# Kernel tuning notes

Measured on AMD Instinct MI355X. Metric: run time of the kernel, lower is better.

Reference implementation:

```python
import jax, jax.numpy as jnp
import numpy as np

N, E, IN_DIM, HIDDEN, OUT_DIM, HOPS, NUM_GRAPHS = 50000, 800000, 128, 128, 10, 4, 128


def setup_inputs() -> dict:
    key = jax.random.key(0)
    ks = jax.random.split(key, 10)
    x = jax.random.normal(ks[0], (N, IN_DIM), dtype=jnp.float32)
    edge_index = jax.random.randint(ks[1], (2, E), 0, N, dtype=jnp.int64)
    batch = jnp.sort(jax.random.randint(ks[2], (N,), 0, NUM_GRAPHS, dtype=jnp.int64))
    s = 0.05
    W_in = jax.random.normal(ks[3], (IN_DIM, HIDDEN), dtype=jnp.float32) * s
    b_in = jnp.zeros((HIDDEN,), dtype=jnp.float32)
    W_hops = jax.random.normal(ks[4], (HOPS, HIDDEN, HIDDEN), dtype=jnp.float32) * s
    b_hops = jnp.zeros((HOPS, HIDDEN), dtype=jnp.float32)
    W_cls = jax.random.normal(ks[5], (HIDDEN, OUT_DIM), dtype=jnp.float32) * s
    b_cls = jnp.zeros((OUT_DIM,), dtype=jnp.float32)
    return {"x": x, "edge_index": edge_index, "batch": batch,
            "W_in": W_in, "b_in": b_in, "W_hops": W_hops, "b_hops": b_hops,
            "W_cls": W_cls, "b_cls": b_cls}


def reference(x, edge_index, batch, W_in, b_in, W_hops, b_hops, W_cls, b_cls):
    src, dst = edge_index[0], edge_index[1]
    # LinearEncoder
    h = x @ W_in + b_in
    # GCN symmetric normalization with self-loops (edge weight 1):
    # deg[i] = 1 + in-degree(i)
    deg = 1.0 + jax.ops.segment_sum(jnp.ones((E,), h.dtype), dst, num_segments=N)
    dinv = deg ** -0.5                      # [N]
    edge_norm = (dinv[src] * dinv[dst])[:, None]   # [E,1]
    self_norm = (dinv * dinv)[:, None]             # [N,1]

    def gcn_conv(h, W, b):
        xw = h @ W                                           # [N,H]
        msg = xw[src] * edge_norm                            # gather + scale
        agg = jax.ops.segment_sum(msg, dst, num_segments=N)  # scatter-add
        return agg + xw * self_norm + b

    for i in range(HOPS):
        h = gcn_conv(h, W_hops[i], b_hops[i])
        if i != HOPS - 1:
            h = jax.nn.relu(h)  # dropout is identity in eval mode

    y = h @ W_cls + b_cls                                    # [N,OUT]
    # global mean pool over graphs
    sums = jax.ops.segment_sum(y, batch, num_segments=NUM_GRAPHS)
    cnts = jax.ops.segment_sum(jnp.ones((N,), y.dtype), batch, num_segments=NUM_GRAPHS)
    return sums / jnp.maximum(cnts, 1.0)[:, None]
```

## Files before the change

### kernel.cpp

```cpp
#include <hip/hip_runtime.h>
#include <hip/hip_fp16.h>

#define N_NODES 50000
#define N_EDGES 800000
#define HID 128
#define OUTD 10
#define NGRAPH 128
#define CAP 64
#define OVF_MAX 4096
#define GBM 64
#define EPT 2

typedef __attribute__((ext_vector_type(8))) short short8;
typedef __attribute__((ext_vector_type(4))) float f32x4;

__device__ __forceinline__ int ld_idx(const int* p, int i, int is64) {
  return is64 ? p[2 * i] : p[i];
}

__device__ __forceinline__ void split1(float v, unsigned& hb, unsigned& lb) {
  unsigned u = __float_as_uint(v);
  hb = (u + 0x7FFFu + ((u >> 16) & 1u)) >> 16;
  float r = v - __uint_as_float(hb << 16);
  unsigned ur = __float_as_uint(r);
  lb = (ur + 0x7FFFu + ((ur >> 16) & 1u)) >> 16;
}

__device__ __forceinline__ float4 h4_to_f4(uint2 u) {
  __half2 a = *(__half2*)&u.x;
  __half2 b = *(__half2*)&u.y;
  float2 fa = __half22float2(a);
  float2 fb = __half22float2(b);
  return make_float4(fa.x, fa.y, fb.x, fb.y);
}

__global__ __launch_bounds__(256) void setup_kernel(const int* __restrict__ ei,
                                                    const float* __restrict__ W_in,
                                                    const float* __restrict__ W_hops,
                                                    const float* __restrict__ Wc,
                                                    const float* __restrict__ b4,
                                                    const float* __restrict__ bc,
                                                    int* __restrict__ flag,
                                                    unsigned short* __restrict__ WhiT,
                                                    unsigned short* __restrict__ WloT,
                                                    float* __restrict__ Wf,
                                                    float* __restrict__ bf) {
  int b = blockIdx.x;
  int tid = threadIdx.x;
  if (b == 0) {
    if (tid == 0) {
      int all0 = 1;
      for (int i = 0; i < 64; ++i) {
        if (ei[2 * i + 1] != 0) { all0 = 0; break; }
      }
      flag[0] = all0;
    }
  } else if (b <= 4) {
    int m = b - 1;
    const float* W = (m == 0) ? W_in : (W_hops + (size_t)(m - 1) * HID * HID);
    unsigned short* oh = WhiT + (size_t)m * HID * HID;
    unsigned short* ol = WloT + (size_t)m * HID * HID;
    for (int it = 0; it < 64; ++it) {
      int idx = it * 256 + tid;
      int k = idx >> 7, n = idx & 127;
      unsigned hb, lb;
      split1(W[k * HID + n], hb, lb);
      oh[n * HID + k] = (unsigned short)hb;
      ol[n * HID + k] = (unsigned short)lb;
    }
  } else {
    const float* W4 = W_hops + 3 * (size_t)HID * HID;
    for (int idx = tid; idx < HID * OUTD; idx += 256) {
      int k = idx / OUTD, o = idx % OUTD;
      float s = 0.f;
      for (int j = 0; j < HID; ++j) s += W4[k * HID + j] * Wc[j * OUTD + o];
      Wf[idx] = s;
    }
    if (tid < OUTD) {
      float s = bc[tid];
      for (int j = 0; j < HID; ++j) s += b4[j] * Wc[j * OUTD + tid];
      bf[tid] = s;
    }
  }
}

__global__ __launch_bounds__(256) void ew_kernel(const int* __restrict__ fillcnt,
                                                 const int* __restrict__ col_fixed,
                                                 float* __restrict__ ew) {
  int wave = threadIdx.x >> 6;
  int lane = threadIdx.x & 63;
  int node = blockIdx.x * 4 + wave;
  if (node >= N_NODES) return;
  int deg = fillcnt[node];
  float dd = 1.0f / sqrtf(1.0f + (float)deg);
  int m = min(deg, CAP);
  if (lane < m) {
    int src = col_fixed[node * CAP + lane];
    float ds = 1.0f / sqrtf(1.0f + (float)fillcnt[src]);
    ew[node * CAP + lane] = dd * ds;
  }
}

__device__ __forceinline__ void gemm_mfma_body(const float* __restrict__ A,
                                               const unsigned short* __restrict__ WhT,
                                               const unsigned short* __restrict__ WlT,
                                               const float* __restrict__ bias,
                                               float* __restrict__ C32,
                                               __half* __restrict__ C16,
                                               int M, int row0) {
  __shared__ unsigned short sBall[2 * 64 * HID];
  unsigned short* sBhi = sBall;
  unsigned short* sBlo = sBall + 64 * HID;
  int tid = threadIdx.x;
  int w = tid >> 6, lane = tid & 63;
  int m = lane & 15, kq = lane >> 4;
  int arow = min(row0 + w * 16 + m, M - 1);
  const float* Ap = A + (size_t)arow * HID + kq * 8;

  short8 AH[4], AL[4];
#pragma unroll
  for (int kc4 = 0; kc4 < 4; ++kc4) {
    float4 a0 = *(const float4*)(Ap + kc4 * 32);
    float4 a1 = *(const float4*)(Ap + kc4 * 32 + 4);
    float av[8] = {a0.x, a0.y, a0.z, a0.w, a1.x, a1.y, a1.z, a1.w};
#pragma unroll
    for (int i = 0; i < 8; ++i) {
      unsigned hb, lb;
      split1(av[i], hb, lb);
      AH[kc4][i] = (short)hb;
      AL[kc4][i] = (short)lb;
    }
  }

  f32x4 acc[8];
#pragma unroll
  for (int j = 0; j < 8; ++j) acc[j] = (f32x4){0.f, 0.f, 0.f, 0.f};

#pragma unroll
  for (int half = 0; half < 2; ++half) {
    if (half) __syncthreads();
#pragma unroll
    for (int it = 0; it < 8; ++it) {
      int f = it * 256 + tid;
      int mat = f >> 10;
      int ln = (f >> 4) & 63;
      int c = f & 15;
      int cs = c ^ (ln & 15);
      const unsigned short* src = (mat ? WlT : WhT) + (size_t)(half * 64 + ln) * HID + c * 8;
      unsigned short* dst = (mat ? sBlo : sBhi) + ln * HID + cs * 8;
      *(uint4*)dst = *(const uint4*)src;
    }
    __syncthreads();

#pragma unroll
    for (int kc4 = 0; kc4 < 4; ++kc4) {
      int kc = kc4 * 4 + kq;
      int cs = kc ^ m;
#pragma unroll
      for (int jl = 0; jl < 4; ++jl) {
        int ln = jl * 16 + m;
        short8 bhi = *(const short8*)&sBhi[ln * HID + cs * 8];
        short8 blo = *(const short8*)&sBlo[ln * HID + cs * 8];
        int j = half * 4 + jl;
        acc[j] = __builtin_amdgcn_mfma_f32_16x16x32_bf16(AH[kc4], bhi, acc[j], 0, 0, 0);
        acc[j] = __builtin_amdgcn_mfma_f32_16x16x32_bf16(AL[kc4], bhi, acc[j], 0, 0, 0);
        acc[j] = __builtin_amdgcn_mfma_f32_16x16x32_bf16(AH[kc4], blo, acc[j], 0, 0, 0);
      }
    }
  }

  __syncthreads();
  float* sC = (float*)sBall;
  int rloc = w * 16 + (lane >> 4) * 4;
#pragma unroll
  for (int j = 0; j < 8; ++j) {
    int col = j * 16 + m;
    float bv = bias ? bias[col] : 0.f;
#pragma unroll
    for (int r = 0; r < 4; ++r)
      sC[(rloc + r) * HID + col] = acc[j][r] + bv;
  }
  __syncthreads();
  if (C16) {
#pragma unroll
    for (int it = 0; it < 8; ++it) {
      int f = it * 256 + tid;
      int rr = f >> 5;
      int c4 = (f & 31) * 4;
      int grow = row0 + rr;
      if (grow < M) {
        float4 v = *(const float4*)&sC[rr * HID + c4];
        __half2 h0 = __floats2half2_rn(v.x, v.y);
        __half2 h1 = __floats2half2_rn(v.z, v.w);
        uint2 u;
        u.x = *(unsigned*)&h0;
        u.y = *(unsigned*)&h1;
        *(uint2*)(C16 + (size_t)grow * HID + c4) = u;
      }
    }
  } else {
#pragma unroll
    for (int it = 0; it < 8; ++it) {
      int f = it * 256 + tid;
      int rr = f >> 5;
      int c4 = (f & 31) * 4;
      int grow = row0 + rr;
      if (grow < M) {
        float4 v = *(const float4*)&sC[rr * HID + c4];
        *(float4*)(C32 + (size_t)grow * HID + c4) = v;
      }
    }
  }
}

__global__ __launch_bounds__(256) void gemm_kernel(const float* __restrict__ A,
                                                   const unsigned short* __restrict__ WhT,
                                                   const unsigned short* __restrict__ WlT,
                                                   __half* __restrict__ C16, int M) {
  gemm_mfma_body(A, WhT, WlT, nullptr, nullptr, C16, M, blockIdx.x * GBM);
}

__device__ __forceinline__ void fill_phase(const int* __restrict__ ei,
                                           int* __restrict__ fillcnt,
                                           int* __restrict__ col_fixed,
                                           int* __restrict__ ovf_cnt,
                                           int* __restrict__ ovf,
                                           const int* __restrict__ flag,
                                           int e0, int e1) {
  int is64 = flag[0];
  int tid = threadIdx.x;
  int base = e0 + blockIdx.x * (256 * EPT);
  int dsts[EPT], srcs[EPT], pos[EPT];
#pragma unroll
  for (int u = 0; u < EPT; ++u) {
    int e = base + u * 256 + tid;
    if (e < e1) {
      dsts[u] = ld_idx(ei, N_EDGES + e, is64);
      srcs[u] = ld_idx(ei, e, is64);
    } else {
      dsts[u] = -1; srcs[u] = 0;
    }
  }
#pragma unroll
  for (int u = 0; u < EPT; ++u)
    pos[u] = (dsts[u] >= 0) ? atomicAdd(&fillcnt[dsts[u]], 1) : 0;
#pragma unroll
  for (int u = 0; u < EPT; ++u) {
    if (dsts[u] >= 0) {
      if (pos[u] < CAP) {
        col_fixed[dsts[u] * CAP + pos[u]] = srcs[u];
      } else {
        int o = atomicAdd(ovf_cnt, 1);
        if (o < OVF_MAX) { ovf[2 * o] = dsts[u]; ovf[2 * o + 1] = srcs[u]; }
      }
    }
  }
}

__global__ __launch_bounds__(256) void gemm_fill_kernel(const float* __restrict__ A,
                                                        const unsigned short* __restrict__ WhT,
                                                        const unsigned short* __restrict__ WlT,
                                                        const float* __restrict__ bias,
                                                        float* __restrict__ C32,
                                                        __half* __restrict__ C16,
                                                        const int* __restrict__ ei,
                                                        int* __restrict__ fillcnt,
                                                        int* __restrict__ col_fixed,
                                                        int* __restrict__ ovf_cnt,
                                                        int* __restrict__ ovf,
                                                        const int* __restrict__ flag,
                                                        int e0, int e1) {
  if (blockIdx.x & 1) {
    fill_phase(ei, fillcnt, col_fixed, ovf_cnt, ovf, flag, e0, e1);
    gemm_mfma_body(A, WhT, WlT, bias, C32, C16, N_NODES, blockIdx.x * GBM);
  } else {
    gemm_mfma_body(A, WhT, WlT, bias, C32, C16, N_NODES, blockIdx.x * GBM);
    fill_phase(ei, fillcnt, col_fixed, ovf_cnt, ovf, flag, e0, e1);
  }
}

__global__ __launch_bounds__(256) void agg_kernel(const __half* __restrict__ xw,
                                                  const int* __restrict__ fillcnt,
                                                  const int* __restrict__ col_fixed,
                                                  const float* __restrict__ ew,
                                                  const float* __restrict__ bias,
                                                  const int* __restrict__ ovf_cnt,
                                                  const int* __restrict__ ovf,
                                                  float* __restrict__ out, int relu) {
  int wave = threadIdx.x >> 6;
  int lane = threadIdx.x & 63;
  int node = blockIdx.x * 4 + wave;
  if (node >= N_NODES) return;
  int h = lane >> 5;
  int q = lane & 31;

  const uint2* x2 = (const uint2*)xw;
  int deg = fillcnt[node];
  int m = min(deg, CAP);
  float4 acc = make_float4(0.f, 0.f, 0.f, 0.f);
  if (h == 0) {
    float sn = 1.0f / (1.0f + (float)deg);
    float4 v = h4_to_f4(x2[(size_t)node * 32 + q]);
    float4 b = ((const float4*)bias)[q];
    acc.x = v.x * sn + b.x; acc.y = v.y * sn + b.y;
    acc.z = v.z * sn + b.z; acc.w = v.w * sn + b.w;
  }

  int cidx = node;
  float cw = 0.f;
  if (lane < m) {
    cidx = col_fixed[node * CAP + lane];
    cw = ew[node * CAP + lane];
  }

#define AGG_FETCH(P, BUF, WBUF)                                                         \
  {                                                                                     \
    int _pa = (P) < 62 ? (P) : 62;                                                      \
    int _s0 = __builtin_amdgcn_readlane(cidx, _pa);                                     \
    int _s1 = __builtin_amdgcn_readlane(cidx, _pa + 1);                                 \
    float _wa = __uint_as_float((unsigned)__builtin_amdgcn_readlane((int)__float_as_uint(cw), _pa));     \
    float _wb = __uint_as_float((unsigned)__builtin_amdgcn_readlane((int)__float_as_uint(cw), _pa + 1)); \
    int _srcp = h ? _s1 : _s0;                                                          \
    WBUF = h ? _wb : _wa;                                                               \
    BUF = x2[(size_t)_srcp * 32 + q];                                                   \
  }

  if (m > 0) {
    uint2 b0, b1, b2;
    float w0, w1, w2;
    AGG_FETCH(0, b0, w0);
    AGG_FETCH(2, b1, w1);
    AGG_FETCH(4, b2, w2);
    for (int jj = 0; jj < m; jj += 2) {
      float4 u = h4_to_f4(b0);
      acc.x += u.x * w0; acc.y += u.y * w0;
      acc.z += u.z * w0; acc.w += u.w * w0;
      b0 = b1; w0 = w1;
      b1 = b2; w1 = w2;
      AGG_FETCH(jj + 6, b2, w2);
    }
  }
#undef AGG_FETCH

  if (deg > CAP && h == 0) {
    int novf = min(*ovf_cnt, OVF_MAX);
    float dd = rsqrtf(1.0f + (float)deg);
    for (int o = 0; o < novf; ++o) {
      if (ovf[2 * o] == node) {
        int src = ovf[2 * o + 1];
        float w = rsqrtf(1.0f + (float)fillcnt[src]) * dd;
        float4 u = h4_to_f4(x2[(size_t)src * 32 + q]);
        acc.x += u.x * w; acc.y += u.y * w;
        acc.z += u.z * w; acc.w += u.w * w;
      }
    }
  }

  acc.x += __shfl_xor(acc.x, 32, 64);
  acc.y += __shfl_xor(acc.y, 32, 64);
  acc.z += __shfl_xor(acc.z, 32, 64);
  acc.w += __shfl_xor(acc.w, 32, 64);

  if (h == 0) {
    if (relu) {
      acc.x = fmaxf(acc.x, 0.f); acc.y = fmaxf(acc.y, 0.f);
      acc.z = fmaxf(acc.z, 0.f); acc.w = fmaxf(acc.w, 0.f);
    }
    ((float4*)out)[(size_t)node * 32 + q] = acc;
  }
}

__global__ __launch_bounds__(256) void z_kernel(const float* __restrict__ h,
                                                const float* __restrict__ Wf,
                                                float* __restrict__ z, int M) {
  __shared__ float sW[HID * OUTD];
  int tid = threadIdx.x;
  for (int i = tid; i < HID * OUTD; i += 256) sW[i] = Wf[i];
  __syncthreads();
  int row = blockIdx.x * 256 + tid;
  if (row >= M) return;
  float y[OUTD];
#pragma unroll
  for (int o = 0; o < OUTD; ++o) y[o] = 0.f;
  const float4* hr = (const float4*)(h + (size_t)row * HID);
  for (int k4 = 0; k4 < 32; ++k4) {
    float4 hv = hr[k4];
    int kb = k4 * 4;
#pragma unroll
    for (int o = 0; o < OUTD; ++o) {
      y[o] += hv.x * sW[(kb + 0) * OUTD + o];
      y[o] += hv.y * sW[(kb + 1) * OUTD + o];
      y[o] += hv.z * sW[(kb + 2) * OUTD + o];
      y[o] += hv.w * sW[(kb + 3) * OUTD + o];
    }
  }
#pragma unroll
  for (int o = 0; o < OUTD; ++o) z[(size_t)row * OUTD + o] = y[o];
}

__global__ __launch_bounds__(256) void agg10_kernel(const float* __restrict__ z,
                                                    const int* __restrict__ fillcnt,
                                                    const int* __restrict__ col_fixed,
                                                    const float* __restrict__ ew,
                                                    const float* __restrict__ bf,
                                                    const int* __restrict__ ovf_cnt,
                                                    const int* __restrict__ ovf,
                                                    const int* __restrict__ batch,
                                                    float* __restrict__ pool,
                                                    float* __restrict__ cnt,
                                                    const int* __restrict__ flag) {
  __shared__ float spool[NGRAPH * OUTD];
  __shared__ float scount[NGRAPH];
  int tid = threadIdx.x;
  for (int i = tid; i < NGRAPH * OUTD; i += 256) spool[i] = 0.f;
  if (tid < NGRAPH) scount[tid] = 0.f;
  __syncthreads();

  int is64 = flag[0];
  int node = blockIdx.x * 256 + tid;
  bool valid = node < N_NODES;
  int nc = valid ? node : (N_NODES - 1);
  int g = ld_idx(batch, nc, is64);

  float acc[OUTD];
#pragma unroll
  for (int o = 0; o < OUTD; ++o) acc[o] = 0.f;
  float c = 0.f;

  if (valid) {
    int deg = fillcnt[node];
    float sn = 1.0f / (1.0f + (float)deg);
#pragma unroll
    for (int o = 0; o < OUTD; ++o) acc[o] = z[(size_t)node * OUTD + o] * sn + bf[o];
    c = 1.f;

    int m = min(deg, CAP);
    for (int j = 0; j < m; ++j) {
      int src = col_fixed[node * CAP + j];
      float w = ew[node * CAP + j];
      const float2* zr = (const float2*)(z + (size_t)src * OUTD);
#pragma unroll
      for (int p = 0; p < 5; ++p) {
        float2 u = zr[p];
        acc[2 * p] += u.x * w;
        acc[2 * p + 1] += u.y * w;
      }
    }
    if (deg > CAP) {
      int novf = min(*ovf_cnt, OVF_MAX);
      float dd = rsqrtf(1.0f + (float)deg);
      for (int o = 0; o < novf; ++o) {
        if (ovf[2 * o] == node) {
          int src = ovf[2 * o + 1];
          float w = rsqrtf(1.0f + (float)fillcnt[src]) * dd;
#pragma unroll
          for (int qq = 0; qq < OUTD; ++qq) acc[qq] += z[(size_t)src * OUTD + qq] * w;
        }
      }
    }
  }

  int g0 = __builtin_amdgcn_readfirstlane(g);
  unsigned long long same = __ballot(g == g0);
  unsigned long long act = __ballot(1);
  if (same == act) {
#pragma unroll
    for (int off = 1; off < 64; off <<= 1) {
#pragma unroll
      for (int o = 0; o < OUTD; ++o) acc[o] += __shfl_xor(acc[o], off, 64);
      c += __shfl_xor(c, off, 64);
    }
    if ((tid & 63) == 0) {
#pragma unroll
      for (int o = 0; o < OUTD; ++o) atomicAdd(&spool[g0 * OUTD + o], acc[o]);
      atomicAdd(&scount[g0], c);
    }
  } else if (valid) {
#pragma unroll
    for (int o = 0; o < OUTD; ++o) atomicAdd(&spool[g * OUTD + o], acc[o]);
    atomicAdd(&scount[g], 1.f);
  }
  __syncthreads();
  for (int i = tid; i < NGRAPH * OUTD; i += 256) {
    float v = spool[i];
    if (v != 0.f) atomicAdd(&pool[i], v);
  }
  if (tid < NGRAPH && scount[tid] != 0.f) atomicAdd(&cnt[tid], scount[tid]);
}

__global__ void finalize_kernel(const float* __restrict__ pool,
                                const float* __restrict__ cnt,
                                float* __restrict__ out) {
  int i = blockIdx.x * blockDim.x + threadIdx.x;
  if (i < NGRAPH * OUTD) {
    float c = cnt[i / OUTD];
    out[i] = pool[i] / fmaxf(c, 1.0f);
  }
}

extern "C" void kernel_launch(void* const* d_in, const int* in_sizes, int n_in,
                              void* d_out, int out_size, void* d_ws, size_t ws_size,
                              hipStream_t stream) {
  const float* x      = (const float*)d_in[0];
  const int*   ei     = (const int*)d_in[1];
  const int*   batch  = (const int*)d_in[2];
  const float* W_in   = (const float*)d_in[3];
  const float* b_in   = (const float*)d_in[4];
  const float* W_hops = (const float*)d_in[5];
  const float* b_hops = (const float*)d_in[6];
  const float* W_cls  = (const float*)d_in[7];
  const float* b_cls  = (const float*)d_in[8];
  float* out = (float*)d_out;

  char* ws = (char*)d_ws;
  size_t off = 0;
  auto alloc = [&](size_t bytes) -> void* {
    void* p = ws + off;
    off += (bytes + 255) & ~(size_t)255;
    return p;
  };

  int*   fillcnt = (int*)alloc(N_NODES * 4);
  int*   ovf_cnt = (int*)alloc(4);
  float* pool    = (float*)alloc(NGRAPH * OUTD * 4);
  float* cnt     = (float*)alloc(NGRAPH * 4);
  size_t zero_bytes = off;
  int*   flag    = (int*)alloc(4);
  int*   ovf     = (int*)alloc(OVF_MAX * 2 * 4);
  int*   col_fixed = (int*)alloc((size_t)N_NODES * CAP * 4);
  float* ew      = (float*)alloc((size_t)N_NODES * CAP * 4);
  float* bufA    = (float*)alloc((size_t)N_NODES * HID * 4);
  __half* bufB   = (__half*)alloc((size_t)N_NODES * HID * 2);
  float* z       = (float*)alloc((size_t)N_NODES * OUTD * 4);
  float* Wf      = (float*)alloc(HID * OUTD * 4);
  float* bf      = (float*)alloc(16 * 4);
  unsigned short* WhiT = (unsigned short*)alloc(4 * HID * HID * 2);
  unsigned short* WloT = (unsigned short*)alloc(4 * HID * HID * 2);
  (void)ws_size; (void)in_sizes; (void)n_in; (void)out_size;

  hipMemsetAsync(d_ws, 0, zero_bytes, stream);
  setup_kernel<<<6, 256, 0, stream>>>(ei, W_in, W_hops, W_cls,
                                      b_hops + 3 * HID, b_cls,
                                      flag, WhiT, WloT, Wf, bf);

  const int gblocks = (N_NODES + GBM - 1) / GBM;
  const int EHALF = N_EDGES / 2;
  const int WW = HID * HID;

  gemm_fill_kernel<<<gblocks, 256, 0, stream>>>(x, WhiT, WloT, b_in, bufA, nullptr,
                                                ei, fillcnt, col_fixed, ovf_cnt, ovf, flag,
                                                0, EHALF);
  gemm_fill_kernel<<<gblocks, 256, 0, stream>>>(bufA, WhiT + WW, WloT + WW, nullptr,
                                                nullptr, bufB,
                                                ei, fillcnt, col_fixed, ovf_cnt, ovf, flag,
                                                EHALF, N_EDGES);
  ew_kernel<<<(N_NODES + 3) / 4, 256, 0, stream>>>(fillcnt, col_fixed, ew);

  agg_kernel<<<(N_NODES + 3) / 4, 256, 0, stream>>>(bufB, fillcnt, col_fixed, ew,
                                                    b_hops, ovf_cnt, ovf, bufA, 1);
  for (int i = 1; i < 3; ++i) {
    gemm_kernel<<<gblocks, 256, 0, stream>>>(bufA, WhiT + (size_t)(i + 1) * WW,
                                             WloT + (size_t)(i + 1) * WW, bufB, N_NODES);
    agg_kernel<<<(N_NODES + 3) / 4, 256, 0, stream>>>(bufB, fillcnt, col_fixed, ew,
                                                      b_hops + (size_t)i * HID, ovf_cnt, ovf,
                                                      bufA, 1);
  }

  int nb = (N_NODES + 255) / 256;
  z_kernel<<<nb, 256, 0, stream>>>(bufA, Wf, z, N_NODES);
  agg10_kernel<<<nb, 256, 0, stream>>>(z, fillcnt, col_fixed, ew, bf,
                                       ovf_cnt, ovf, batch, pool, cnt, flag);
  finalize_kernel<<<(NGRAPH * OUTD + 255) / 256, 256, 0, stream>>>(pool, cnt, out);
}
```

Baseline: 367.0 us.

## Fuse edge-weight and classifier projection into aggregation, store activations in fp16

The separate edge-weight kernel is removed. The first aggregation now computes the normalized edge weights inline and writes them out for later hops. The last aggregation is fused with the classifier projection through a wave-level shuffle reduction, which removes the z_kernel and its round trip of the full hidden activations. Intermediate activations between hops are stored as fp16 instead of fp32, halving that memory traffic, at some cost in precision on the hidden states fed to the next GEMM.

After: 376.3 us. 2.5% more time.

```diff
diff --git a/kernel.cpp b/kernel.cpp
--- a/kernel.cpp
+++ b/kernel.cpp
@@ -84,28 +84,11 @@
   }
 }
 
-__global__ __launch_bounds__(256) void ew_kernel(const int* __restrict__ fillcnt,
-                                                 const int* __restrict__ col_fixed,
-                                                 float* __restrict__ ew) {
-  int wave = threadIdx.x >> 6;
-  int lane = threadIdx.x & 63;
-  int node = blockIdx.x * 4 + wave;
-  if (node >= N_NODES) return;
-  int deg = fillcnt[node];
-  float dd = 1.0f / sqrtf(1.0f + (float)deg);
-  int m = min(deg, CAP);
-  if (lane < m) {
-    int src = col_fixed[node * CAP + lane];
-    float ds = 1.0f / sqrtf(1.0f + (float)fillcnt[src]);
-    ew[node * CAP + lane] = dd * ds;
-  }
-}
-
-__device__ __forceinline__ void gemm_mfma_body(const float* __restrict__ A,
+template <bool A16>
+__device__ __forceinline__ void gemm_mfma_body(const void* __restrict__ Av,
                                                const unsigned short* __restrict__ WhT,
                                                const unsigned short* __restrict__ WlT,
                                                const float* __restrict__ bias,
-                                               float* __restrict__ C32,
                                                __half* __restrict__ C16,
                                                int M, int row0) {
   __shared__ unsigned short sBall[2 * 64 * HID];
@@ -115,14 +98,25 @@
   int w = tid >> 6, lane = tid & 63;
   int m = lane & 15, kq = lane >> 4;
   int arow = min(row0 + w * 16 + m, M - 1);
-  const float* Ap = A + (size_t)arow * HID + kq * 8;
 
   short8 AH[4], AL[4];
 #pragma unroll
   for (int kc4 = 0; kc4 < 4; ++kc4) {
-    float4 a0 = *(const float4*)(Ap + kc4 * 32);
-    float4 a1 = *(const float4*)(Ap + kc4 * 32 + 4);
-    float av[8] = {a0.x, a0.y, a0.z, a0.w, a1.x, a1.y, a1.z, a1.w};
+    float av[8];
+    if (A16) {
+      const __half* Ap = (const __half*)Av + (size_t)arow * HID + kq * 8;
+      uint4 raw = *(const uint4*)(Ap + kc4 * 32);
+      float4 f0 = h4_to_f4(make_uint2(raw.x, raw.y));
+      float4 f1 = h4_to_f4(make_uint2(raw.z, raw.w));
+      av[0] = f0.x; av[1] = f0.y; av[2] = f0.z; av[3] = f0.w;
+      av[4] = f1.x; av[5] = f1.y; av[6] = f1.z; av[7] = f1.w;
+    } else {
+      const float* Ap = (const float*)Av + (size_t)arow * HID + kq * 8;
+      float4 a0 = *(const float4*)(Ap + kc4 * 32);
+      float4 a1 = *(const float4*)(Ap + kc4 * 32 + 4);
+      av[0] = a0.x; av[1] = a0.y; av[2] = a0.z; av[3] = a0.w;
+      av[4] = a1.x; av[5] = a1.y; av[6] = a1.z; av[7] = a1.w;
+    }
 #pragma unroll
     for (int i = 0; i < 8; ++i) {
       unsigned hb, lb;
@@ -181,43 +175,30 @@
       sC[(rloc + r) * HID + col] = acc[j][r] + bv;
   }
   __syncthreads();
-  if (C16) {
-#pragma unroll
-    for (int it = 0; it < 8; ++it) {
-      int f = it * 256 + tid;
-      int rr = f >> 5;
-      int c4 = (f & 31) * 4;
-      int grow = row0 + rr;
-      if (grow < M) {
-        float4 v = *(const float4*)&sC[rr * HID + c4];
-        __half2 h0 = __floats2half2_rn(v.x, v.y);
-        __half2 h1 = __floats2half2_rn(v.z, v.w);
-        uint2 u;
-        u.x = *(unsigned*)&h0;
-        u.y = *(unsigned*)&h1;
-        *(uint2*)(C16 + (size_t)grow * HID + c4) = u;
-      }
-    }
-  } else {
-#pragma unroll
-    for (int it = 0; it < 8; ++it) {
-      int f = it * 256 + tid;
-      int rr = f >> 5;
-      int c4 = (f & 31) * 4;
-      int grow = row0 + rr;
-      if (grow < M) {
-        float4 v = *(const float4*)&sC[rr * HID + c4];
-        *(float4*)(C32 + (size_t)grow * HID + c4) = v;
-      }
-    }
-  }
-}
-
-__global__ __launch_bounds__(256) void gemm_kernel(const float* __restrict__ A,
+#pragma unroll
+  for (int it = 0; it < 8; ++it) {
+    int f = it * 256 + tid;
+    int rr = f >> 5;
+    int c4 = (f & 31) * 4;
+    int grow = row0 + rr;
+    if (grow < M) {
+      float4 v = *(const float4*)&sC[rr * HID + c4];
+      __half2 h0 = __floats2half2_rn(v.x, v.y);
+      __half2 h1 = __floats2half2_rn(v.z, v.w);
+      uint2 u;
+      u.x = *(unsigned*)&h0;
+      u.y = *(unsigned*)&h1;
+      *(uint2*)(C16 + (size_t)grow * HID + c4) = u;
+    }
+  }
+}
+
+template <bool A16>
+__global__ __launch_bounds__(256) void gemm_kernel(const void* __restrict__ A,
                                                    const unsigned short* __restrict__ WhT,
                                                    const unsigned short* __restrict__ WlT,
                                                    __half* __restrict__ C16, int M) {
-  gemm_mfma_body(A, WhT, WlT, nullptr, nullptr, C16, M, blockIdx.x * GBM);
+  gemm_mfma_body<A16>(A, WhT, WlT, nullptr, C16, M, blockIdx.x * GBM);
 }
 
 __device__ __forceinline__ void fill_phase(const int* __restrict__ ei,
@@ -257,11 +238,11 @@
   }
 }
 
-__global__ __launch_bounds__(256) void gemm_fill_kernel(const float* __restrict__ A,
+template <bool A16>
+__global__ __launch_bounds__(256) void gemm_fill_kernel(const void* __restrict__ A,
                                                         const unsigned short* __restrict__ WhT,
                                                         const unsigned short* __restrict__ WlT,
                                                         const float* __restrict__ bias,
-                                                        float* __restrict__ C32,
                                                         __half* __restrict__ C16,
                                                         const int* __restrict__ ei,
                                                         int* __restrict__ fillcnt,
@@ -272,34 +253,29 @@
                                                         int e0, int e1) {
   if (blockIdx.x & 1) {
     fill_phase(ei, fillcnt, col_fixed, ovf_cnt, ovf, flag, e0, e1);
-    gemm_mfma_body(A, WhT, WlT, bias, C32, C16, N_NODES, blockIdx.x * GBM);
+    gemm_mfma_body<A16>(A, WhT, WlT, bias, C16, N_NODES, blockIdx.x * GBM);
   } else {
-    gemm_mfma_body(A, WhT, WlT, bias, C32, C16, N_NODES, blockIdx.x * GBM);
+    gemm_mfma_body<A16>(A, WhT, WlT, bias, C16, N_NODES, blockIdx.x * GBM);
     fill_phase(ei, fillcnt, col_fixed, ovf_cnt, ovf, flag, e0, e1);
   }
 }
 
-__global__ __launch_bounds__(256) void agg_kernel(const __half* __restrict__ xw,
-                                                  const int* __restrict__ fillcnt,
-                                                  const int* __restrict__ col_fixed,
-                                                  const float* __restrict__ ew,
-                                                  const float* __restrict__ bias,
-                                                  const int* __restrict__ ovf_cnt,
-                                                  const int* __restrict__ ovf,
-                                                  float* __restrict__ out, int relu) {
-  int wave = threadIdx.x >> 6;
-  int lane = threadIdx.x & 63;
-  int node = blockIdx.x * 4 + wave;
-  if (node >= N_NODES) return;
-  int h = lane >> 5;
-  int q = lane & 31;
-
+template <bool FIRST>
+__device__ __forceinline__ float4 gather_body(int node, int lane, int h, int q,
+                                              const __half* __restrict__ xw,
+                                              const int* __restrict__ fillcnt,
+                                              const int* __restrict__ col_fixed,
+                                              float* __restrict__ ew,
+                                              const float* __restrict__ bias,
+                                              const int* __restrict__ ovf_cnt,
+                                              const int* __restrict__ ovf) {
   const uint2* x2 = (const uint2*)xw;
   int deg = fillcnt[node];
   int m = min(deg, CAP);
   float4 acc = make_float4(0.f, 0.f, 0.f, 0.f);
+  float dd = rsqrtf(1.0f + (float)deg);
   if (h == 0) {
-    float sn = 1.0f / (1.0f + (float)deg);
+    float sn = dd * dd;
     float4 v = h4_to_f4(x2[(size_t)node * 32 + q]);
     float4 b = ((const float4*)bias)[q];
     acc.x = v.x * sn + b.x; acc.y = v.y * sn + b.y;
@@ -310,7 +286,12 @@
   float cw = 0.f;
   if (lane < m) {
     cidx = col_fixed[node * CAP + lane];
-    cw = ew[node * CAP + lane];
+    if (FIRST) {
+      cw = rsqrtf(1.0f + (float)fillcnt[cidx]) * dd;
+      ew[node * CAP + lane] = cw;
+    } else {
+      cw = ew[node * CAP + lane];
+    }
   }
 
 #define AGG_FETCH(P, BUF, WBUF)                                                         \
@@ -344,7 +325,6 @@
 
   if (deg > CAP && h == 0) {
     int novf = min(*ovf_cnt, OVF_MAX);
-    float dd = rsqrtf(1.0f + (float)deg);
     for (int o = 0; o < novf; ++o) {
       if (ovf[2 * o] == node) {
         int src = ovf[2 * o + 1];
@@ -360,42 +340,83 @@
   acc.y += __shfl_xor(acc.y, 32, 64);
   acc.z += __shfl_xor(acc.z, 32, 64);
   acc.w += __shfl_xor(acc.w, 32, 64);
-
+  return acc;
+}
+
+template <bool FIRST>
+__global__ __launch_bounds__(256) void agg_kernel(const __half* __restrict__ xw,
+                                                  const int* __restrict__ fillcnt,
+                                                  const int* __restrict__ col_fixed,
+                                                  float* __restrict__ ew,
+                                                  const float* __restrict__ bias,
+                                                  const int* __restrict__ ovf_cnt,
+                                                  const int* __restrict__ ovf,
+                                                  __half* __restrict__ out) {
+  int wave = threadIdx.x >> 6;
+  int lane = threadIdx.x & 63;
+  int node = blockIdx.x * 4 + wave;
+  if (node >= N_NODES) return;
+  int h = lane >> 5;
+  int q = lane & 31;
+
+  float4 acc = gather_body<FIRST>(node, lane, h, q, xw, fillcnt, col_fixed, ew,
+                                  bias, ovf_cnt, ovf);
   if (h == 0) {
-    if (relu) {
-      acc.x = fmaxf(acc.x, 0.f); acc.y = fmaxf(acc.y, 0.f);
-      acc.z = fmaxf(acc.z, 0.f); acc.w = fmaxf(acc.w, 0.f);
-    }
-    ((float4*)out)[(size_t)node * 32 + q] = acc;
-  }
-}
-
-__global__ __launch_bounds__(256) void z_kernel(const float* __restrict__ h,
-                                                const float* __restrict__ Wf,
-                                                float* __restrict__ z, int M) {
-  __shared__ float sW[HID * OUTD];
+    acc.x = fmaxf(acc.x, 0.f); acc.y = fmaxf(acc.y, 0.f);
+    acc.z = fmaxf(acc.z, 0.f); acc.w = fmaxf(acc.w, 0.f);
+    __half2 h0 = __floats2half2_rn(acc.x, acc.y);
+    __half2 h1 = __floats2half2_rn(acc.z, acc.w);
+    uint2 u;
+    u.x = *(unsigned*)&h0;
+    u.y = *(unsigned*)&h1;
+    ((uint2*)out)[(size_t)node * 32 + q] = u;
+  }
+}
+
+__global__ __launch_bounds__(256) void agg_z_kernel(const __half* __restrict__ xw,
+                                                    const int* __restrict__ fillcnt,
+                                                    const int* __restrict__ col_fixed,
+                                                    float* __restrict__ ew,
+                                                    const float* __restrict__ bias,
+                                                    const int* __restrict__ ovf_cnt,
+                                                    const int* __restrict__ ovf,
+                                                    const float* __restrict__ Wf,
+                                                    float* __restrict__ z) {
+  __shared__ float sWf[HID * OUTD];
   int tid = threadIdx.x;
-  for (int i = tid; i < HID * OUTD; i += 256) sW[i] = Wf[i];
+  for (int i = tid; i < HID * OUTD; i += 256) sWf[i] = Wf[i];
   __syncthreads();
-  int row = blockIdx.x * 256 + tid;
-  if (row >= M) return;
-  float y[OUTD];
-#pragma unroll
-  for (int o = 0; o < OUTD; ++o) y[o] = 0.f;
-  const float4* hr = (const float4*)(h + (size_t)row * HID);
-  for (int k4 = 0; k4 < 32; ++k4) {
-    float4 hv = hr[k4];
-    int kb = k4 * 4;
-#pragma unroll
-    for (int o = 0; o < OUTD; ++o) {
-      y[o] += hv.x * sW[(kb + 0) * OUTD + o];
-      y[o] += hv.y * sW[(kb + 1) * OUTD + o];
-      y[o] += hv.z * sW[(kb + 2) * OUTD + o];
-      y[o] += hv.w * sW[(kb + 3) * OUTD + o];
-    }
-  }
-#pragma unroll
-  for (int o = 0; o < OUTD; ++o) z[(size_t)row * OUTD + o] = y[o];
+
+  int wave = tid >> 6;
+  int lane = tid & 63;
+  int node = blockIdx.x * 4 + wave;
+  if (node >= N_NODES) return;
+  int h = lane >> 5;
+  int q = lane & 31;
+
+  float4 acc = gather_body<false>(node, lane, h, q, xw, fillcnt, col_fixed, ew,
+                                  bias, ovf_cnt, ovf);
+  acc.x = fmaxf(acc.x, 0.f); acc.y = fmaxf(acc.y, 0.f);
+  acc.z = fmaxf(acc.z, 0.f); acc.w = fmaxf(acc.w, 0.f);
+
+  float p[OUTD];
+#pragma unroll
+  for (int o = 0; o < OUTD; ++o) {
+    p[o] = acc.x * sWf[(4 * q + 0) * OUTD + o]
+         + acc.y * sWf[(4 * q + 1) * OUTD + o]
+         + acc.z * sWf[(4 * q + 2) * OUTD + o]
+         + acc.w * sWf[(4 * q + 3) * OUTD + o];
+  }
+#pragma unroll
+  for (int off = 1; off < 32; off <<= 1) {
+#pragma unroll
+    for (int o = 0; o < OUTD; ++o) p[o] += __shfl_xor(p[o], off, 64);
+  }
+  if (lane == 0) {
+    float2* zr = (float2*)(z + (size_t)node * OUTD);
+#pragma unroll
+    for (int pr = 0; pr < 5; ++pr) zr[pr] = make_float2(p[2 * pr], p[2 * pr + 1]);
+  }
 }
 
 __global__ __launch_bounds__(256) void agg10_kernel(const float* __restrict__ z,
@@ -529,8 +550,8 @@
   int*   ovf     = (int*)alloc(OVF_MAX * 2 * 4);
   int*   col_fixed = (int*)alloc((size_t)N_NODES * CAP * 4);
   float* ew      = (float*)alloc((size_t)N_NODES * CAP * 4);
-  float* bufA    = (float*)alloc((size_t)N_NODES * HID * 4);
-  __half* bufB   = (__half*)alloc((size_t)N_NODES * HID * 2);
+  __half* bufH   = (__half*)alloc((size_t)N_NODES * HID * 2);
+  __half* bufX   = (__half*)alloc((size_t)N_NODES * HID * 2);
   float* z       = (float*)alloc((size_t)N_NODES * OUTD * 4);
   float* Wf      = (float*)alloc(HID * OUTD * 4);
   float* bf      = (float*)alloc(16 * 4);
@@ -544,30 +565,28 @@
                                       flag, WhiT, WloT, Wf, bf);
 
   const int gblocks = (N_NODES + GBM - 1) / GBM;
+  const int ablocks = (N_NODES + 3) / 4;
   const int EHALF = N_EDGES / 2;
   const int WW = HID * HID;
 
-  gemm_fill_kernel<<<gblocks, 256, 0, stream>>>(x, WhiT, WloT, b_in, bufA, nullptr,
-                                                ei, fillcnt, col_fixed, ovf_cnt, ovf, flag,
-                                                0, EHALF);
-  gemm_fill_kernel<<<gblocks, 256, 0, stream>>>(bufA, WhiT + WW, WloT + WW, nullptr,
-                                                nullptr, bufB,
-                                                ei, fillcnt, col_fixed, ovf_cnt, ovf, flag,
-                                                EHALF, N_EDGES);
-  ew_kernel<<<(N_NODES + 3) / 4, 256, 0, stream>>>(fillcnt, col_fixed, ew);
-
-  agg_kernel<<<(N_NODES + 3) / 4, 256, 0, stream>>>(bufB, fillcnt, col_fixed, ew,
-                                                    b_hops, ovf_cnt, ovf, bufA, 1);
-  for (int i = 1; i < 3; ++i) {
-    gemm_kernel<<<gblocks, 256, 0, stream>>>(bufA, WhiT + (size_t)(i + 1) * WW,
-                                             WloT + (size_t)(i + 1) * WW, bufB, N_NODES);
-    agg_kernel<<<(N_NODES + 3) / 4, 256, 0, stream>>>(bufB, fillcnt, col_fixed, ew,
-                                                      b_hops + (size_t)i * HID, ovf_cnt, ovf,
-                                                      bufA, 1);
-  }
-
+  gemm_fill_kernel<false><<<gblocks, 256, 0, stream>>>(x, WhiT, WloT, b_in, bufH,
+                                                       ei, fillcnt, col_fixed, ovf_cnt, ovf,
+                                                       flag, 0, EHALF);
+  gemm_fill_kernel<true><<<gblocks, 256, 0, stream>>>(bufH, WhiT + WW, WloT + WW, nullptr,
+                                                      bufX,
+                                                      ei, fillcnt, col_fixed, ovf_cnt, ovf,
+                                                      flag, EHALF, N_EDGES);
+  agg_kernel<true><<<ablocks, 256, 0, stream>>>(bufX, fillcnt, col_fixed, ew,
+                                                b_hops, ovf_cnt, ovf, bufH);
+  gemm_kernel<true><<<gblocks, 256, 0, stream>>>(bufH, WhiT + 2 * WW, WloT + 2 * WW,
+                                                 bufX, N_NODES);
+  agg_kernel<false><<<ablocks, 256, 0, stream>>>(bufX, fillcnt, col_fixed, ew,
+                                                 b_hops + HID, ovf_cnt, ovf, bufH);
+  gemm_kernel<true><<<gblocks, 256, 0, stream>>>(bufH, WhiT + 3 * WW, WloT + 3 * WW,
+                                                 bufX, N_NODES);
+  agg_z_kernel<<<ablocks, 256, 0, stream>>>(bufX, fillcnt, col_fixed, ew,
+                                            b_hops + 2 * HID, ovf_cnt, ovf, Wf, z);
   int nb = (N_NODES + 255) / 256;
-  z_kernel<<<nb, 256, 0, stream>>>(bufA, Wf, z, N_NODES);
   agg10_kernel<<<nb, 256, 0, stream>>>(z, fillcnt, col_fixed, ew, bf,
                                        ovf_cnt, ovf, batch, pool, cnt, flag);
   finalize_kernel<<<(NGRAPH * OUTD + 255) / 256, 256, 0, stream>>>(pool, cnt, out);
```
